# Performance work log

Measured on AMD Instinct MI355X. Metric: run time of the kernel, lower is better.

The kernel has to match this reference:

```python
import jax, jax.numpy as jnp
import numpy as np

B, S, T = 512, 1024, 48  # batch, seq_len, num_tags


def setup_inputs() -> dict:
    key = jax.random.key(0)
    k1, k2, k3, k4, k5, k6 = jax.random.split(key, 6)
    emissions = jax.random.normal(k1, (B, S, T), dtype=jnp.float32)
    tags = jax.random.randint(k2, (B, S), 0, T)
    lengths = jax.random.randint(k3, (B,), 1, S + 1)
    mask = jnp.arange(S)[None, :] < lengths[:, None]  # contiguous prefix mask, bool
    # learned parameters (nn.Parameter zeros init in the module; use small random here)
    start_transitions = 0.01 * jax.random.normal(k4, (T,), dtype=jnp.float32)
    end_transitions = 0.01 * jax.random.normal(k5, (T,), dtype=jnp.float32)
    transitions = 0.01 * jax.random.normal(k6, (T, T), dtype=jnp.float32)
    return {
        "emissions": emissions,
        "tags": tags,
        "mask": mask,
        "start_transitions": start_transitions,
        "end_transitions": end_transitions,
        "transitions": transitions,
    }


def _log_partition(emissions, mask, start_transitions, end_transitions, transitions):
    # score[b, i] = log-sum over paths ending in tag i (note: this repo indexes
    # transitions[i, j] with j = previous tag inside the partition recursion).
    score0 = start_transitions[None, :] + emissions[:, 0]  # (B, T)

    def step(score, xs):
        emit_t, mask_t = xs  # (B, T), (B,)
        # score_t[b, i] = logsumexp_j(score[b, j] + transitions[i, j]) + emit_t[b, i]
        score_t = jax.nn.logsumexp(score[:, None, :] + transitions[None, :, :], axis=2) + emit_t
        score = jnp.where(mask_t[:, None], score_t, score)
        return score, None

    em = jnp.swapaxes(emissions[:, 1:], 0, 1)  # (S-1, B, T)
    mk = jnp.swapaxes(mask[:, 1:], 0, 1)       # (S-1, B)
    score, _ = jax.lax.scan(step, score0, (em, mk))
    return jax.nn.logsumexp(score + end_transitions[None, :], axis=1)  # (B,)


def _score_sentence(emissions, tags, mask, start_transitions, end_transitions, transitions):
    Bb = emissions.shape[0]
    bidx = jnp.arange(Bb)
    maskf = mask.astype(emissions.dtype)
    score = start_transitions[tags[:, 0]] + emissions[bidx, 0, tags[:, 0]]  # (B,)
    trans_sc = transitions[tags[:, :-1], tags[:, 1:]]  # (B, S-1)
    emit_sc = jnp.take_along_axis(emissions, tags[:, :, None], axis=2)[..., 0]  # (B, S)
    score = score + jnp.sum((trans_sc + emit_sc[:, 1:]) * maskf[:, 1:], axis=1)
    last_idx = jnp.sum(mask.astype(jnp.int32), axis=1) - 1  # (B,)
    last_tags = jnp.take_along_axis(tags, last_idx[:, None], axis=1)[:, 0]
    return score + end_transitions[last_tags]


def reference(emissions, tags, mask, start_transitions, end_transitions, transitions):
    log_denominator = _log_partition(emissions, mask, start_transitions, end_transitions, transitions)
    log_numerator = _score_sentence(emissions, tags, mask, start_transitions, end_transitions, transitions)
    return jnp.mean(log_denominator - log_numerator)
```

## Files before the change

kernel.cpp:

```cpp
#include <hip/hip_runtime.h>

#define BB 512
#define SS 1024
#define TT 48
#define GG 16
#define CK 8
#define NSLOT 5

typedef __attribute__((ext_vector_type(8))) short short8;
typedef __attribute__((ext_vector_type(4))) float float4v;

__device__ __forceinline__ unsigned short f2bf(float x) {
    unsigned u = __float_as_uint(x);
    u += 0x7FFFu + ((u >> 16) & 1u);
    return (unsigned short)(u >> 16);
}
__device__ __forceinline__ unsigned pk2bf(float lo, float hi) {
#if __has_builtin(__builtin_amdgcn_cvt_pk_bf16_f32)
    typedef __bf16 bf16x2 __attribute__((ext_vector_type(2)));
    union { bf16x2 v; unsigned u; } cv;
    cv.v = __builtin_amdgcn_cvt_pk_bf16_f32(lo, hi);
    return cv.u;
#else
    return __builtin_amdgcn_perm(__float_as_uint(hi) + 0x8000u,
                                 __float_as_uint(lo) + 0x8000u, 0x07060302u);
#endif
}
__device__ __forceinline__ float bflo(unsigned u) { return __uint_as_float(u << 16); }
__device__ __forceinline__ float bfhi(unsigned u) { return __uint_as_float(u & 0xFFFF0000u); }
__device__ __forceinline__ float wave_sum(float v) {
#pragma unroll
    for (int off = 32; off >= 1; off >>= 1) v += __shfl_xor(v, off, 64);
    return v;
}
__device__ __forceinline__ int wave_sum_i(int v) {
#pragma unroll
    for (int off = 32; off >= 1; off >>= 1) v += __shfl_xor(v, off, 64);
    return v;
}

__global__ __launch_bounds__(256)
void crf_numer(const float* __restrict__ em, const int* __restrict__ tags,
               const int* __restrict__ mask, const float* __restrict__ start_tr,
               const float* __restrict__ end_tr, const float* __restrict__ trans,
               float* __restrict__ numer, int* __restrict__ lenArr) {
    const int b = blockIdx.x, tid = threadIdx.x;
    const float* emb = em + (size_t)b * SS * TT;
    const int* tg = tags + (size_t)b * SS;
    const int* mk = mask + (size_t)b * SS;
    int cnt = 0; float ns = 0.f;
    for (int s = tid; s < SS; s += 256) {
        int m = mk[s];
        cnt += (m != 0);
        if (s >= 1 && m) {
            int tp = tg[s - 1], tc = tg[s];
            ns += trans[tp * TT + tc] + emb[s * TT + tc];
        }
    }
    float wsum = wave_sum(ns);
    int wcnt = wave_sum_i(cnt);
    __shared__ float sf[4]; __shared__ int si[4];
    if ((tid & 63) == 0) { sf[tid >> 6] = wsum; si[tid >> 6] = wcnt; }
    __syncthreads();
    if (tid == 0) {
        float tot = sf[0] + sf[1] + sf[2] + sf[3];
        int L = si[0] + si[1] + si[2] + si[3];
        int t0 = tg[0];
        tot += start_tr[t0] + emb[t0] + end_tr[tg[L - 1]];
        numer[b] = tot;
        lenArr[b] = L;
    }
}

__global__ __launch_bounds__(256)
void crf_fwd(const float* __restrict__ em, const float* __restrict__ start_tr,
             const float* __restrict__ end_tr, const float* __restrict__ trans,
             const int* __restrict__ lenArr, float* __restrict__ denomArr) {
    __shared__ uint2 ring[NSLOT * CK * 3 * 64];

    const int tid = threadIdx.x;
    const int wave = tid >> 6, lane = tid & 63;
    const int wgbase = blockIdx.x * GG;

    if (wave == 0) {
        const int n = lane & 15, q = lane >> 4;
        const int bb = wgbase + n;
        const int ec = n * 4 + q;

        short8 afr[3][2];
#pragma unroll
        for (int mt = 0; mt < 3; ++mt) {
            const int so = mt * 16 + n;
#pragma unroll
            for (int kt = 0; kt < 2; ++kt) {
                short8 a;
#pragma unroll
                for (int i = 0; i < 8; ++i) {
                    int si_;
                    if (kt == 0) si_ = (i < 4) ? (q * 4 + i) : (16 + q * 4 + (i - 4));
                    else         si_ = (i < 4) ? (32 + q * 4 + i) : -1;
                    a[i] = (si_ >= 0) ? (short)f2bf(__expf(trans[so * TT + si_])) : (short)0;
                }
                afr[mt][kt] = a;
            }
        }

        const float* em0 = em + (size_t)bb * SS * TT + q * 4;
        float p[3][4];
#pragma unroll
        for (int mt = 0; mt < 3; ++mt) {
            float4 v = *(const float4*)(em0 + mt * 16);
            int sb = mt * 16 + q * 4;
            p[mt][0] = __expf(start_tr[sb + 0] + v.x);
            p[mt][1] = __expf(start_tr[sb + 1] + v.y);
            p[mt][2] = __expf(start_tr[sb + 2] + v.z);
            p[mt][3] = __expf(start_tr[sb + 3] + v.w);
        }

        const int len = lenArr[bb];
        int Lmax = len;
#pragma unroll
        for (int off = 1; off < 64; off <<= 1) {
            int o = __shfl_xor(Lmax, off, 64);
            Lmax = Lmax > o ? Lmax : o;
        }
        const int P = (Lmax + 6) >> 3;

        bool cc0 = (len == 1);
        float dc[3][4];
#pragma unroll
        for (int mt = 0; mt < 3; ++mt)
#pragma unroll
            for (int r = 0; r < 4; ++r) dc[mt][r] = cc0 ? p[mt][r] : 0.f;
        float lcap = 0.f, logscale = 0.f;
        const float4v Z = {0.f, 0.f, 0.f, 0.f};

        for (int pp = -3; pp < P; ++pp) {
            if (pp >= 0) {
                const uint2* rp = &ring[(pp % NSLOT) * (CK * 3 * 64) + ec];
                uint2 c0 = rp[0], c1 = rp[64], c2v = rp[128];
#pragma unroll
                for (int u = 0; u < 8; ++u) {
                    uint2 n0, n1, n2;
                    if (u < 7) {
                        n0 = rp[(u + 1) * 192];
                        n1 = rp[(u + 1) * 192 + 64];
                        n2 = rp[(u + 1) * 192 + 128];
                    }
                    union { short8 v; unsigned w[4]; } B0, B1;
                    B0.w[0] = pk2bf(p[0][0], p[0][1]); B0.w[1] = pk2bf(p[0][2], p[0][3]);
                    B0.w[2] = pk2bf(p[1][0], p[1][1]); B0.w[3] = pk2bf(p[1][2], p[1][3]);
                    B1.w[0] = pk2bf(p[2][0], p[2][1]); B1.w[1] = pk2bf(p[2][2], p[2][3]);
                    B1.w[2] = 0u; B1.w[3] = 0u;
                    float4v A0 = __builtin_amdgcn_mfma_f32_16x16x32_bf16(afr[0][0], B0.v, Z, 0, 0, 0);
                    float4v A1 = __builtin_amdgcn_mfma_f32_16x16x32_bf16(afr[1][0], B0.v, Z, 0, 0, 0);
                    float4v A2 = __builtin_amdgcn_mfma_f32_16x16x32_bf16(afr[2][0], B0.v, Z, 0, 0, 0);
                    A0 = __builtin_amdgcn_mfma_f32_16x16x32_bf16(afr[0][1], B1.v, A0, 0, 0, 0);
                    A1 = __builtin_amdgcn_mfma_f32_16x16x32_bf16(afr[1][1], B1.v, A1, 0, 0, 0);
                    A2 = __builtin_amdgcn_mfma_f32_16x16x32_bf16(afr[2][1], B1.v, A2, 0, 0, 0);
                    p[0][0] = A0[0] * bflo(c0.x); p[0][1] = A0[1] * bfhi(c0.x);
                    p[0][2] = A0[2] * bflo(c0.y); p[0][3] = A0[3] * bfhi(c0.y);
                    p[1][0] = A1[0] * bflo(c1.x); p[1][1] = A1[1] * bfhi(c1.x);
                    p[1][2] = A1[2] * bflo(c1.y); p[1][3] = A1[3] * bfhi(c1.y);
                    p[2][0] = A2[0] * bflo(c2v.x); p[2][1] = A2[1] * bfhi(c2v.x);
                    p[2][2] = A2[2] * bflo(c2v.y); p[2][3] = A2[3] * bfhi(c2v.y);
                    bool cc = (len == 8 * pp + u + 2);
#pragma unroll
                    for (int mt = 0; mt < 3; ++mt)
#pragma unroll
                        for (int r = 0; r < 4; ++r) dc[mt][r] = cc ? p[mt][r] : dc[mt][r];
                    lcap = cc ? logscale : lcap;
                    c0 = n0; c1 = n1; c2v = n2;
                    if (u == 7) {
                        float m = fmaxf(p[0][0], p[0][1]);
                        m = fmaxf(m, fmaxf(p[0][2], p[0][3]));
                        m = fmaxf(m, fmaxf(p[1][0], p[1][1]));
                        m = fmaxf(m, fmaxf(p[1][2], p[1][3]));
                        m = fmaxf(m, fmaxf(p[2][0], p[2][1]));
                        m = fmaxf(m, fmaxf(p[2][2], p[2][3]));
                        m = fmaxf(m, __shfl_xor(m, 16, 64));
                        m = fmaxf(m, __shfl_xor(m, 32, 64));
                        m = fmaxf(m, 1e-30f);
                        logscale += __logf(m);
                        float rm = __builtin_amdgcn_rcpf(m);
#pragma unroll
                        for (int mt = 0; mt < 3; ++mt)
#pragma unroll
                            for (int r = 0; r < 4; ++r) p[mt][r] *= rm;
                    }
                }
            }
            __builtin_amdgcn_s_barrier();
        }

        float pe = 0.f;
#pragma unroll
        for (int mt = 0; mt < 3; ++mt) {
            int sb = mt * 16 + q * 4;
            pe = fmaf(dc[mt][0], __expf(end_tr[sb + 0]), pe);
            pe = fmaf(dc[mt][1], __expf(end_tr[sb + 1]), pe);
            pe = fmaf(dc[mt][2], __expf(end_tr[sb + 2]), pe);
            pe = fmaf(dc[mt][3], __expf(end_tr[sb + 3]), pe);
        }
        pe += __shfl_xor(pe, 16, 64);
        pe += __shfl_xor(pe, 32, 64);
        if (lane < 16) denomArr[bb] = lcap + __logf(pe);

    } else {
        const int my = wave - 1;
        const int nb = lane >> 2, q4 = lane & 3;
        const int bb = wgbase + nb;
        const int len_v = lenArr[bb];
        int Lmax = len_v;
#pragma unroll
        for (int off = 1; off < 64; off <<= 1) {
            int o = __shfl_xor(Lmax, off, 64);
            Lmax = Lmax > o ? Lmax : o;
        }
        const int P = (Lmax + 6) >> 3;

        const float* emP = em + (size_t)bb * SS * TT + q4 * 4;
        float4 buf[CK][3];

        for (int pp = -3; pp < P; ++pp) {
            int c1 = pp + 3;
            if (c1 < P && (c1 % 3) == my) {
                if (8 * c1 + 8 <= SS - 1) {
                    const float* cb = emP + (size_t)(1 + 8 * c1) * TT;
#pragma unroll
                    for (int u = 0; u < CK; ++u)
#pragma unroll
                        for (int j = 0; j < 3; ++j)
                            buf[u][j] = *(const float4*)(cb + u * TT + j * 16);
                } else {
#pragma unroll
                    for (int u = 0; u < CK; ++u) {
                        int t = 1 + 8 * c1 + u; t = t < SS ? t : SS - 1;
#pragma unroll
                        for (int j = 0; j < 3; ++j)
                            buf[u][j] = *(const float4*)(emP + (size_t)t * TT + j * 16);
                    }
                }
            }
            int c2 = pp + 1;
            if (c2 >= 0 && c2 < P && (c2 % 3) == my) {
                uint2* wp = &ring[(c2 % NSLOT) * (CK * 3 * 64) + lane];
#pragma unroll
                for (int u = 0; u < CK; ++u) {
                    int t = 1 + 8 * c2 + u;
                    bool live = t < len_v;
#pragma unroll
                    for (int j = 0; j < 3; ++j) {
                        float4 v = buf[u][j];
                        unsigned lox = pk2bf(__expf(v.x), __expf(v.y));
                        unsigned hix = pk2bf(__expf(v.z), __expf(v.w));
                        uint2 o;
                        o.x = live ? lox : 0u;
                        o.y = live ? hix : 0u;
                        wp[u * 192 + j * 64] = o;
                    }
                }
            }
            __builtin_amdgcn_s_waitcnt(0xC07F);
            __builtin_amdgcn_s_barrier();
        }
    }
}

__global__ __launch_bounds__(64)
void crf_reduce(const float* __restrict__ denom, const float* __restrict__ numer,
                float* __restrict__ out) {
    int lane = threadIdx.x;
    float s = 0.f;
    for (int i = lane; i < BB; i += 64) s += denom[i] - numer[i];
    s = wave_sum(s);
    if (lane == 0) out[0] = s * (1.0f / (float)BB);
}

extern "C" void kernel_launch(void* const* d_in, const int* in_sizes, int n_in,
                              void* d_out, int out_size, void* d_ws, size_t ws_size,
                              hipStream_t stream) {
    const float* emissions = (const float*)d_in[0];
    const int*   tags      = (const int*)d_in[1];
    const int*   mask      = (const int*)d_in[2];
    const float* start_tr  = (const float*)d_in[3];
    const float* end_tr    = (const float*)d_in[4];
    const float* trans     = (const float*)d_in[5];

    char* ws = (char*)d_ws;
    float* denom = (float*)ws;
    float* numer = (float*)(ws + 2048);
    int*   lenA  = (int*)(ws + 4096);

    crf_numer<<<BB, 256, 0, stream>>>(emissions, tags, mask, start_tr, end_tr,
                                      trans, numer, lenA);
    crf_fwd<<<BB / GG, 256, 0, stream>>>(emissions, start_tr, end_tr, trans,
                                         lenA, denom);
    crf_reduce<<<1, 64, 0, stream>>>(denom, numer, (float*)d_out);
}
```

Measured before the change: 322.1 us.

## Split emission producers into four waves sharing alternating chunks and remap ring layout

The forward kernel grows from 4 to 5 waves. The emission-loading waves are reorganised into two teams of two: each team handles every other chunk, and each wave loads and converts half of a chunk (12 float4s instead of 24). This halves the per-wave register buffer. Lane mapping changes so the batch index is lane&15, which lets the MFMA consumer read the ring at offset lane instead of a permuted index. Loads for a future chunk are now issued after the ring write for the current one, which may change latency hiding.

```diff
diff --git a/kernel.cpp b/kernel.cpp
--- a/kernel.cpp
+++ b/kernel.cpp
@@ -72,7 +72,7 @@
     }
 }
 
-__global__ __launch_bounds__(256)
+__global__ __launch_bounds__(320, 1)
 void crf_fwd(const float* __restrict__ em, const float* __restrict__ start_tr,
              const float* __restrict__ end_tr, const float* __restrict__ trans,
              const int* __restrict__ lenArr, float* __restrict__ denomArr) {
@@ -85,7 +85,6 @@
     if (wave == 0) {
         const int n = lane & 15, q = lane >> 4;
         const int bb = wgbase + n;
-        const int ec = n * 4 + q;
 
         short8 afr[3][2];
 #pragma unroll
@@ -137,7 +136,7 @@
 
         for (int pp = -3; pp < P; ++pp) {
             if (pp >= 0) {
-                const uint2* rp = &ring[(pp % NSLOT) * (CK * 3 * 64) + ec];
+                const uint2* rp = &ring[(pp % NSLOT) * (CK * 3 * 64) + lane];
                 uint2 c0 = rp[0], c1 = rp[64], c2v = rp[128];
 #pragma unroll
                 for (int u = 0; u < 8; ++u) {
@@ -207,8 +206,9 @@
         if (lane < 16) denomArr[bb] = lcap + __logf(pe);
 
     } else {
-        const int my = wave - 1;
-        const int nb = lane >> 2, q4 = lane & 3;
+        const int T = (wave - 1) >> 1;
+        const int sub = (wave - 1) & 1;
+        const int nb = lane & 15, q4 = lane >> 4;
         const int bb = wgbase + nb;
         const int len_v = lenArr[bb];
         int Lmax = len_v;
@@ -220,45 +220,33 @@
         const int P = (Lmax + 6) >> 3;
 
         const float* emP = em + (size_t)bb * SS * TT + q4 * 4;
-        float4 buf[CK][3];
+        float4 buf[12];
 
         for (int pp = -3; pp < P; ++pp) {
-            int c1 = pp + 3;
-            if (c1 < P && (c1 % 3) == my) {
-                if (8 * c1 + 8 <= SS - 1) {
-                    const float* cb = emP + (size_t)(1 + 8 * c1) * TT;
-#pragma unroll
-                    for (int u = 0; u < CK; ++u)
-#pragma unroll
-                        for (int j = 0; j < 3; ++j)
-                            buf[u][j] = *(const float4*)(cb + u * TT + j * 16);
-                } else {
-#pragma unroll
-                    for (int u = 0; u < CK; ++u) {
-                        int t = 1 + 8 * c1 + u; t = t < SS ? t : SS - 1;
-#pragma unroll
-                        for (int j = 0; j < 3; ++j)
-                            buf[u][j] = *(const float4*)(emP + (size_t)t * TT + j * 16);
-                    }
-                }
-            }
-            int c2 = pp + 1;
-            if (c2 >= 0 && c2 < P && (c2 % 3) == my) {
-                uint2* wp = &ring[(c2 % NSLOT) * (CK * 3 * 64) + lane];
-#pragma unroll
-                for (int u = 0; u < CK; ++u) {
-                    int t = 1 + 8 * c2 + u;
+            int cv = pp + 1;
+            if (cv >= 0 && cv < P && (cv & 1) == T) {
+                uint2* wp = &ring[(cv % NSLOT) * (CK * 3 * 64) + lane];
+#pragma unroll
+                for (int k = 0; k < 12; ++k) {
+                    const int i = sub * 12 + k, u = i / 3, j = i % 3;
+                    int t = 1 + 8 * cv + u;
                     bool live = t < len_v;
-#pragma unroll
-                    for (int j = 0; j < 3; ++j) {
-                        float4 v = buf[u][j];
-                        unsigned lox = pk2bf(__expf(v.x), __expf(v.y));
-                        unsigned hix = pk2bf(__expf(v.z), __expf(v.w));
-                        uint2 o;
-                        o.x = live ? lox : 0u;
-                        o.y = live ? hix : 0u;
-                        wp[u * 192 + j * 64] = o;
-                    }
+                    float4 v = buf[k];
+                    unsigned ox = pk2bf(__expf(v.x), __expf(v.y));
+                    unsigned oy = pk2bf(__expf(v.z), __expf(v.w));
+                    uint2 o;
+                    o.x = live ? ox : 0u;
+                    o.y = live ? oy : 0u;
+                    wp[u * 192 + j * 64] = o;
+                }
+            }
+            int ci = pp + 3;
+            if (ci < P && (ci & 1) == T) {
+#pragma unroll
+                for (int k = 0; k < 12; ++k) {
+                    const int i = sub * 12 + k, u = i / 3, j = i % 3;
+                    int t = 1 + 8 * ci + u; t = t < SS ? t : SS - 1;
+                    buf[k] = *(const float4*)(emP + (size_t)t * TT + j * 16);
                 }
             }
             __builtin_amdgcn_s_waitcnt(0xC07F);
@@ -294,7 +282,7 @@
 
     crf_numer<<<BB, 256, 0, stream>>>(emissions, tags, mask, start_tr, end_tr,
                                       trans, numer, lenA);
-    crf_fwd<<<BB / GG, 256, 0, stream>>>(emissions, start_tr, end_tr, trans,
+    crf_fwd<<<BB / GG, 320, 0, stream>>>(emissions, start_tr, end_tr, trans,
                                          lenA, denom);
     crf_reduce<<<1, 64, 0, stream>>>(denom, numer, (float*)d_out);
 }
```

After: 321.6 us. No clear change (-0.2%).
